# Optimization experiments

Hardware: AMD Instinct MI355X
Metric: run time of the kernel (lower is better)

Reference implementation:

```python
import jax, jax.numpy as jnp
import numpy as np

NUM_HEADS = 4
LN_EPS = 1e-5


def setup_inputs() -> dict:
    key = jax.random.key(0)
    ks = jax.random.split(key, 5)
    C = 256
    x = jax.random.normal(ks[0], (2, C, 64, 64), dtype=jnp.float32)
    in_proj_w = jax.random.normal(ks[1], (3 * C, C), dtype=jnp.float32) * (1.0 / np.sqrt(C))
    in_proj_b = jax.random.normal(ks[2], (3 * C,), dtype=jnp.float32) * 0.02
    out_w = jax.random.normal(ks[3], (C, C), dtype=jnp.float32) * (1.0 / np.sqrt(C))
    out_b = jax.random.normal(ks[4], (C,), dtype=jnp.float32) * 0.02
    ln_g = jnp.ones((C,), dtype=jnp.float32)
    ln_b = jnp.zeros((C,), dtype=jnp.float32)
    return {"x": x, "in_proj_w": in_proj_w, "in_proj_b": in_proj_b,
            "out_w": out_w, "out_b": out_b, "ln_g": ln_g, "ln_b": ln_b}


def reference(x, in_proj_w, in_proj_b, out_w, out_b, ln_g, ln_b):
    b, c, H, W = x.shape
    S = H * W  # 4096 == max_tokens -> no pooling, no interpolation
    hd = c // NUM_HEADS
    t = x.reshape(b, c, S).transpose(0, 2, 1)  # (b, S, c)
    # fused QKV projection (in_proj_weight is [3c, c], rows = q,k,v blocks)
    qkv = t @ in_proj_w.T + in_proj_b  # (b, S, 3c)
    q, k, v = jnp.split(qkv, 3, axis=-1)
    def to_heads(a):
        return a.reshape(b, S, NUM_HEADS, hd).transpose(0, 2, 1, 3)  # (b, h, S, d)
    q = to_heads(q) * (1.0 / np.sqrt(hd))
    k = to_heads(k)
    v = to_heads(v)
    scores = jnp.einsum('bhqd,bhkd->bhqk', q, k)      # (b, h, S, S)
    probs = jax.nn.softmax(scores, axis=-1)
    attn = jnp.einsum('bhqk,bhkd->bhqd', probs, v)    # (b, h, S, d)
    attn = attn.transpose(0, 2, 1, 3).reshape(b, S, c)
    out = attn @ out_w.T + out_b                      # output projection
    # LayerNorm over channel dim
    mu = jnp.mean(out, axis=-1, keepdims=True)
    var = jnp.mean(jnp.square(out - mu), axis=-1, keepdims=True)
    out = (out - mu) * jax.lax.rsqrt(var + LN_EPS) * ln_g + ln_b
    return out.transpose(0, 2, 1).reshape(b, c, H, W)
```

## Files before the change

kernel.cpp:

```cpp
#include <hip/hip_runtime.h>
#include <cstddef>

#define S_TOK 4096
#define CDIM 256
#define NHEADS 4
#define HDIM 64
#define LSK 72
#define LDA 36
#define LDY 264
#define LOG2E 1.44269504f

typedef __attribute__((ext_vector_type(8))) short short8;
typedef __attribute__((ext_vector_type(4))) float floatx4;

__device__ inline unsigned short f2bf(float f) {
  union { float f; unsigned u; } v;
  v.f = f;
  unsigned r = v.u + 0x7fff + ((v.u >> 16) & 1);
  return (unsigned short)(r >> 16);
}
__device__ inline float bf2f(unsigned short u) {
  union { unsigned u; float f; } v;
  v.u = ((unsigned)u) << 16;
  return v.f;
}
__device__ inline unsigned pack_bf16(float a, float b) {
#if __has_builtin(__builtin_amdgcn_cvt_pk_bf16_f32)
  typedef __bf16 bf16x2 __attribute__((ext_vector_type(2)));
  union { bf16x2 v; unsigned u; } r;
  r.v = __builtin_amdgcn_cvt_pk_bf16_f32(a, b);
  return r.u;
#else
  return ((unsigned)f2bf(b) << 16) | f2bf(a);
#endif
}

__global__ __launch_bounds__(256) void qkv_gemm_kernel(
    const float* __restrict__ x, const float* __restrict__ ipw,
    const float* __restrict__ ipb, unsigned short* __restrict__ q16,
    unsigned short* __restrict__ k16, unsigned short* __restrict__ vt16) {
  __shared__ __align__(16) unsigned short As[64 * LDA];
  __shared__ __align__(16) unsigned short Bs[3][64 * LDA];
  const int tid = threadIdx.x;
  const int wave = tid >> 6, lane = tid & 63;
  const int quad = lane >> 4, l16 = lane & 15;
  const int n0 = blockIdx.x * 64;
  const int tok0 = blockIdx.y * 64;
  const int b = blockIdx.z;

  const int c_l = tid >> 3, t8 = tid & 7;
  const float* gx = x + (((size_t)(b * CDIM + c_l)) << 12) + tok0 + t8 * 8;
  unsigned short* wa = &As[(t8 * 8) * LDA + c_l];

  const int rr = tid >> 2, c4 = tid & 3;
  const float* gw0 = ipw + ((size_t)(n0 + rr)) * CDIM + c4 * 8;
  unsigned short* wb0 = &Bs[0][rr * LDA + c4 * 8];

  floatx4 acc[3][4];
#pragma unroll
  for (int s = 0; s < 3; ++s)
#pragma unroll
    for (int nt = 0; nt < 4; ++nt) acc[s][nt] = (floatx4){0.f, 0.f, 0.f, 0.f};

  float4 a0 = *(const float4*)(gx);
  float4 a1 = *(const float4*)(gx + 4);
  float4 bp[3][2];
#pragma unroll
  for (int s = 0; s < 3; ++s) {
    bp[s][0] = *(const float4*)(gw0 + (size_t)s * 256 * CDIM);
    bp[s][1] = *(const float4*)(gw0 + (size_t)s * 256 * CDIM + 4);
  }

  for (int ks = 0; ks < 8; ++ks) {
    __syncthreads();
    {
      unsigned p;
      p = pack_bf16(a0.x, a0.y);
      wa[0 * LDA] = (unsigned short)p; wa[1 * LDA] = (unsigned short)(p >> 16);
      p = pack_bf16(a0.z, a0.w);
      wa[2 * LDA] = (unsigned short)p; wa[3 * LDA] = (unsigned short)(p >> 16);
      p = pack_bf16(a1.x, a1.y);
      wa[4 * LDA] = (unsigned short)p; wa[5 * LDA] = (unsigned short)(p >> 16);
      p = pack_bf16(a1.z, a1.w);
      wa[6 * LDA] = (unsigned short)p; wa[7 * LDA] = (unsigned short)(p >> 16);
    }
#pragma unroll
    for (int s = 0; s < 3; ++s) {
      uint2 u0, u1;
      u0.x = pack_bf16(bp[s][0].x, bp[s][0].y);
      u0.y = pack_bf16(bp[s][0].z, bp[s][0].w);
      u1.x = pack_bf16(bp[s][1].x, bp[s][1].y);
      u1.y = pack_bf16(bp[s][1].z, bp[s][1].w);
      unsigned short* w = wb0 + s * 64 * LDA;
      *(uint2*)w = u0;
      *(uint2*)(w + 4) = u1;
    }
    __syncthreads();
    if (ks < 7) {
      const float* gxn = gx + ((size_t)((ks + 1) * 32) << 12);
      a0 = *(const float4*)(gxn);
      a1 = *(const float4*)(gxn + 4);
#pragma unroll
      for (int s = 0; s < 3; ++s) {
        const float* g = gw0 + (size_t)s * 256 * CDIM + (ks + 1) * 32;
        bp[s][0] = *(const float4*)(g);
        bp[s][1] = *(const float4*)(g + 4);
      }
    }
    short8 af = *(const short8*)&As[(wave * 16 + l16) * LDA + quad * 8];
#pragma unroll
    for (int s = 0; s < 3; ++s)
#pragma unroll
      for (int nt = 0; nt < 4; ++nt) {
        short8 bf = *(const short8*)&Bs[s][(nt * 16 + l16) * LDA + quad * 8];
        acc[s][nt] = __builtin_amdgcn_mfma_f32_16x16x32_bf16(af, bf, acc[s][nt], 0, 0, 0);
      }
  }

  const float qsc = 0.125f * LOG2E;
#pragma unroll
  for (int nt = 0; nt < 4; ++nt) {
    int cb = n0 + nt * 16 + l16;
    int h = cb >> 6, dh = cb & 63;
    float bq = ipb[cb], bk = ipb[256 + cb], bv = ipb[512 + cb];
    size_t base = ((size_t)(b * NHEADS + h)) * S_TOK;
#pragma unroll
    for (int r = 0; r < 4; ++r) {
      int tok = tok0 + wave * 16 + quad * 4 + r;
      q16[(base + tok) * HDIM + dh] = f2bf((acc[0][nt][r] + bq) * qsc);
      k16[(base + tok) * HDIM + dh] = f2bf(acc[1][nt][r] + bk);
    }
    int tokv = tok0 + wave * 16 + quad * 4;
    uint2 u;
    u.x = pack_bf16(acc[2][nt][0] + bv, acc[2][nt][1] + bv);
    u.y = pack_bf16(acc[2][nt][2] + bv, acc[2][nt][3] + bv);
    *(uint2*)&vt16[(base * 0 + ((size_t)(b * NHEADS + h) * HDIM + dh)) * S_TOK + tokv] = u;
  }
}

__global__ __launch_bounds__(256) void attn_kernel(
    const unsigned short* __restrict__ q16,
    const unsigned short* __restrict__ k16,
    const unsigned short* __restrict__ vt16,
    unsigned short* __restrict__ op, float* __restrict__ lp) {
  __shared__ __align__(16) unsigned short Ks[64 * LSK];
  __shared__ __align__(16) unsigned short Vt[64 * LSK];
  __shared__ __align__(16) unsigned short Ps[4 * 64 * LSK];

  const int tid = threadIdx.x;
  const int wave = tid >> 6;
  const int lane = tid & 63;
  const int quad = lane >> 4;
  const int l16 = lane & 15;
  const int bh = blockIdx.y;
  const int q0 = blockIdx.x * 256;
  const int split = blockIdx.z;
  const int kt0 = split * 16;

  short8 qf[4][2];
#pragma unroll
  for (int mt = 0; mt < 4; ++mt) {
    const unsigned short* qg =
        q16 + ((size_t)bh * S_TOK + q0 + wave * 64 + mt * 16 + l16) * HDIM + quad * 8;
    qf[mt][0] = *(const short8*)(qg);
    qf[mt][1] = *(const short8*)(qg + 32);
  }

  const int sr = tid >> 3, scc = tid & 7;
  const unsigned short* kg = k16 + ((size_t)bh * S_TOK + sr) * HDIM + scc * 8;
  const unsigned short* vg = vt16 + ((size_t)bh * HDIM + sr) * S_TOK + scc * 8;
  unsigned short* ksw = &Ks[sr * LSK + scc * 8];
  unsigned short* vtw = &Vt[sr * LSK + scc * 8];

  floatx4 O[4][4];
  float lsum[4] = {0.f, 0.f, 0.f, 0.f};
#pragma unroll
  for (int mt = 0; mt < 4; ++mt)
#pragma unroll
    for (int nt = 0; nt < 4; ++nt) O[mt][nt] = (floatx4){0.f, 0.f, 0.f, 0.f};

  uint4 k0r = *(const uint4*)(kg + (size_t)kt0 * 64 * HDIM);
  uint4 k1r = *(const uint4*)(kg + (size_t)kt0 * 64 * HDIM + 32 * HDIM);
  uint4 v0r = *(const uint4*)(vg + kt0 * 64);
  uint4 v1r = *(const uint4*)(vg + kt0 * 64 + (size_t)32 * S_TOK);

  unsigned short* pw = &Ps[(wave * 64) * LSK];

  for (int t = 0; t < 16; ++t) {
    __syncthreads();
    *(uint4*)ksw = k0r;
    *(uint4*)(ksw + 32 * LSK) = k1r;
    *(uint4*)vtw = v0r;
    *(uint4*)(vtw + 32 * LSK) = v1r;
    __syncthreads();
    if (t < 15) {
      const unsigned short* kgn = kg + (size_t)(kt0 + t + 1) * 64 * HDIM;
      const unsigned short* vgn = vg + (kt0 + t + 1) * 64;
      k0r = *(const uint4*)(kgn);
      k1r = *(const uint4*)(kgn + 32 * HDIM);
      v0r = *(const uint4*)(vgn);
      v1r = *(const uint4*)(vgn + (size_t)32 * S_TOK);
    }

#pragma unroll
    for (int kt = 0; kt < 4; ++kt) {
      short8 kf0 = *(const short8*)(&Ks[(kt * 16 + l16) * LSK + quad * 8]);
      short8 kf1 = *(const short8*)(&Ks[(kt * 16 + l16) * LSK + 32 + quad * 8]);
#pragma unroll
      for (int mt = 0; mt < 4; ++mt) {
        floatx4 c = (floatx4){0.f, 0.f, 0.f, 0.f};
        c = __builtin_amdgcn_mfma_f32_16x16x32_bf16(kf0, qf[mt][0], c, 0, 0, 0);
        c = __builtin_amdgcn_mfma_f32_16x16x32_bf16(kf1, qf[mt][1], c, 0, 0, 0);
        float p0 = __builtin_amdgcn_exp2f(c[0]);
        float p1 = __builtin_amdgcn_exp2f(c[1]);
        float p2 = __builtin_amdgcn_exp2f(c[2]);
        float p3 = __builtin_amdgcn_exp2f(c[3]);
        lsum[mt] += (p0 + p1) + (p2 + p3);
        uint2 pk;
        pk.x = pack_bf16(p0, p1);
        pk.y = pack_bf16(p2, p3);
        *(uint2*)&pw[(mt * 16 + l16) * LSK + kt * 16 + quad * 4] = pk;
      }
    }

    short8 pf[4][2];
#pragma unroll
    for (int mt = 0; mt < 4; ++mt) {
      pf[mt][0] = *(const short8*)(&pw[(mt * 16 + l16) * LSK + quad * 8]);
      pf[mt][1] = *(const short8*)(&pw[(mt * 16 + l16) * LSK + 32 + quad * 8]);
    }
#pragma unroll
    for (int nt = 0; nt < 4; ++nt) {
      short8 vf0 = *(const short8*)(&Vt[(nt * 16 + l16) * LSK + quad * 8]);
      short8 vf1 = *(const short8*)(&Vt[(nt * 16 + l16) * LSK + 32 + quad * 8]);
#pragma unroll
      for (int mt = 0; mt < 4; ++mt) {
        O[mt][nt] = __builtin_amdgcn_mfma_f32_16x16x32_bf16(pf[mt][0], vf0, O[mt][nt], 0, 0, 0);
        O[mt][nt] = __builtin_amdgcn_mfma_f32_16x16x32_bf16(pf[mt][1], vf1, O[mt][nt], 0, 0, 0);
      }
    }
  }

  const int b = bh >> 2, h = bh & 3;
  unsigned short* op_s = op + (size_t)split * 2097152;
  float* lp_s = lp + (size_t)split * 32768;
#pragma unroll
  for (int mt = 0; mt < 4; ++mt) {
    float ls = lsum[mt];
    ls += __shfl_xor(ls, 16);
    ls += __shfl_xor(ls, 32);
    if (quad == 0)
      lp_s[bh * S_TOK + q0 + wave * 64 + mt * 16 + l16] = ls;
#pragma unroll
    for (int r = 0; r < 4; ++r) {
      int row = q0 + wave * 64 + mt * 16 + quad * 4 + r;
#pragma unroll
      for (int nt = 0; nt < 4; ++nt)
        op_s[((size_t)(b * S_TOK + row)) * CDIM + h * HDIM + nt * 16 + l16] =
            f2bf(O[mt][nt][r]);
    }
  }
}

__device__ inline uint2 merge4(const unsigned short* op, size_t off, float rinv) {
  float s0 = 0.f, s1 = 0.f, s2 = 0.f, s3 = 0.f;
#pragma unroll
  for (int sp = 0; sp < 4; ++sp) {
    uint2 u = *(const uint2*)(op + (size_t)sp * 2097152 + off);
    s0 += bf2f((unsigned short)(u.x & 0xffff));
    s1 += bf2f((unsigned short)(u.x >> 16));
    s2 += bf2f((unsigned short)(u.y & 0xffff));
    s3 += bf2f((unsigned short)(u.y >> 16));
  }
  uint2 r;
  r.x = pack_bf16(s0 * rinv, s1 * rinv);
  r.y = pack_bf16(s2 * rinv, s3 * rinv);
  return r;
}

__global__ __launch_bounds__(256) void out_ln_gemm_kernel(
    const unsigned short* __restrict__ op, const float* __restrict__ lp,
    const float* __restrict__ ow, const float* __restrict__ obias,
    const float* __restrict__ lng, const float* __restrict__ lnb,
    float* __restrict__ out) {
  __shared__ __align__(16) unsigned short As[32 * LDA];
  __shared__ __align__(16) unsigned short Bs[256 * LDA];
  __shared__ __align__(16) float ys[32 * LDY];
  __shared__ float rsum[128];
  const int tid = threadIdx.x;
  const int wave = tid >> 6, lane = tid & 63;
  const int quad = lane >> 4, l16 = lane & 15;
  const int tok0 = blockIdx.x * 32;

  if (tid < 128) {
    int t = tid >> 2, h = tid & 3;
    int bb = tok0 >> 12;
    int idx = (bb * 4 + h) * 4096 + (tok0 & 4095) + t;
    rsum[tid] =
        1.0f / (lp[idx] + lp[32768 + idx] + lp[65536 + idx] + lp[98304 + idx]);
  }
  __syncthreads();

  const int ar = tid >> 3, ac = tid & 7;
  const size_t abase = (size_t)(tok0 + ar) * CDIM + ac * 4;
  unsigned short* wAp = &As[ar * LDA + ac * 4];
  const int rr = tid >> 2, c4 = tid & 3;
  const float* gB = ow + (size_t)rr * CDIM + c4 * 8;
  unsigned short* wBp = &Bs[rr * LDA + c4 * 8];

  floatx4 acc[2][4];
#pragma unroll
  for (int mt = 0; mt < 2; ++mt)
#pragma unroll
    for (int nt = 0; nt < 4; ++nt) acc[mt][nt] = (floatx4){0.f, 0.f, 0.f, 0.f};

  uint2 ap = merge4(op, abase, rsum[(ar << 2) + (ac >> 4)]);
  float4 bpf[4][2];
#pragma unroll
  for (int i = 0; i < 4; ++i) {
    bpf[i][0] = *(const float4*)(gB + (size_t)i * 64 * CDIM);
    bpf[i][1] = *(const float4*)(gB + (size_t)i * 64 * CDIM + 4);
  }

  for (int ks = 0; ks < 8; ++ks) {
    __syncthreads();
    *(uint2*)wAp = ap;
#pragma unroll
    for (int i = 0; i < 4; ++i) {
      uint2 u0, u1;
      u0.x = pack_bf16(bpf[i][0].x, bpf[i][0].y);
      u0.y = pack_bf16(bpf[i][0].z, bpf[i][0].w);
      u1.x = pack_bf16(bpf[i][1].x, bpf[i][1].y);
      u1.y = pack_bf16(bpf[i][1].z, bpf[i][1].w);
      unsigned short* w = wBp + i * 64 * LDA;
      *(uint2*)w = u0;
      *(uint2*)(w + 4) = u1;
    }
    __syncthreads();
    if (ks < 7) {
      int off = (ks + 1) * 32;
      int ch = off + ac * 4;
      ap = merge4(op, abase + off, rsum[(ar << 2) + (ch >> 6)]);
#pragma unroll
      for (int i = 0; i < 4; ++i) {
        bpf[i][0] = *(const float4*)(gB + (size_t)i * 64 * CDIM + off);
        bpf[i][1] = *(const float4*)(gB + (size_t)i * 64 * CDIM + off + 4);
      }
    }
    short8 af[2], bf[4];
#pragma unroll
    for (int mt = 0; mt < 2; ++mt)
      af[mt] = *(const short8*)&As[(mt * 16 + l16) * LDA + quad * 8];
#pragma unroll
    for (int nt = 0; nt < 4; ++nt)
      bf[nt] = *(const short8*)&Bs[(wave * 64 + nt * 16 + l16) * LDA + quad * 8];
#pragma unroll
    for (int mt = 0; mt < 2; ++mt)
#pragma unroll
      for (int nt = 0; nt < 4; ++nt)
        acc[mt][nt] = __builtin_amdgcn_mfma_f32_16x16x32_bf16(af[mt], bf[nt], acc[mt][nt], 0, 0, 0);
  }

#pragma unroll
  for (int mt = 0; mt < 2; ++mt)
#pragma unroll
    for (int nt = 0; nt < 4; ++nt) {
      int c = wave * 64 + nt * 16 + l16;
      float bo = obias[c];
#pragma unroll
      for (int r = 0; r < 4; ++r)
        ys[(mt * 16 + quad * 4 + r) * LDY + c] = acc[mt][nt][r] + bo;
    }
  __syncthreads();

  const int gtok = tid >> 3, l8 = tid & 7;
  float sum = 0.f, ssq = 0.f;
#pragma unroll
  for (int i = 0; i < 32; ++i) {
    float v = ys[gtok * LDY + i * 8 + l8];
    sum += v;
    ssq += v * v;
  }
  sum += __shfl_xor(sum, 1); ssq += __shfl_xor(ssq, 1);
  sum += __shfl_xor(sum, 2); ssq += __shfl_xor(ssq, 2);
  sum += __shfl_xor(sum, 4); ssq += __shfl_xor(ssq, 4);
  float mu = sum * (1.f / 256.f);
  float var = ssq * (1.f / 256.f) - mu * mu;
  float rstd = rsqrtf(var + 1e-5f);
  const int b2 = tok0 >> 12;
  const int sl = (tok0 & 4095) + gtok;
#pragma unroll
  for (int i = 0; i < 32; ++i) {
    int c = i * 8 + l8;
    float v = ys[gtok * LDY + c];
    out[(((size_t)(b2 * CDIM + c)) << 12) + sl] = (v - mu) * rstd * lng[c] + lnb[c];
  }
}

extern "C" void kernel_launch(void* const* d_in, const int* in_sizes, int n_in,
                              void* d_out, int out_size, void* d_ws, size_t ws_size,
                              hipStream_t stream) {
  const float* x = (const float*)d_in[0];
  const float* ipw = (const float*)d_in[1];
  const float* ipb = (const float*)d_in[2];
  const float* ow = (const float*)d_in[3];
  const float* ob = (const float*)d_in[4];
  const float* lng = (const float*)d_in[5];
  const float* lnb = (const float*)d_in[6];
  float* out = (float*)d_out;
  unsigned short* q16 = (unsigned short*)d_ws;
  unsigned short* k16 = q16 + 2097152;
  unsigned short* vt16 = k16 + 2097152;
  unsigned short* op = vt16 + 2097152;
  float* lp = (float*)(op + 8388608);

  qkv_gemm_kernel<<<dim3(4, 64, 2), 256, 0, stream>>>(x, ipw, ipb, q16, k16, vt16);
  attn_kernel<<<dim3(16, 8, 4), 256, 0, stream>>>(q16, k16, vt16, op, lp);
  out_ln_gemm_kernel<<<256, 256, 0, stream>>>(op, lp, ow, ob, lng, lnb, out);
}
```

Baseline: 150.9 us.

## Keep attention probabilities in registers via permlane swaps and double-buffer K/V

The attention kernel no longer writes the exponentiated scores to a per-wave LDS buffer and reads them back as MFMA operands. It computes two 16-key score tiles, packs them to bf16 and uses v_permlane32/16_swap to rearrange them directly into the A-operand layout for the PV MFMA. K and V tiles are now double-buffered in LDS, with one barrier per iteration instead of two. The fallback pack path also switches to an inline v_cvt_pk_bf16_f32. This removes LDS traffic and a synchronisation point, but relies on gfx950-specific permlane instructions and the correctness of the lane mapping.

Measured after the change: 145.4 us. 3.7% less time.

```diff
diff --git a/kernel.cpp b/kernel.cpp
--- a/kernel.cpp
+++ b/kernel.cpp
@@ -31,8 +31,17 @@
   r.v = __builtin_amdgcn_cvt_pk_bf16_f32(a, b);
   return r.u;
 #else
-  return ((unsigned)f2bf(b) << 16) | f2bf(a);
+  unsigned r;
+  asm("v_cvt_pk_bf16_f32 %0, %1, %2" : "=v"(r) : "v"(a), "v"(b));
+  return r;
 #endif
+}
+
+__device__ inline void pl32swap(unsigned& a, unsigned& b) {
+  asm("v_permlane32_swap_b32 %0, %1" : "+v"(a), "+v"(b));
+}
+__device__ inline void pl16swap(unsigned& a, unsigned& b) {
+  asm("v_permlane16_swap_b32 %0, %1" : "+v"(a), "+v"(b));
 }
 
 __global__ __launch_bounds__(256) void qkv_gemm_kernel(
@@ -143,9 +152,8 @@
     const unsigned short* __restrict__ k16,
     const unsigned short* __restrict__ vt16,
     unsigned short* __restrict__ op, float* __restrict__ lp) {
-  __shared__ __align__(16) unsigned short Ks[64 * LSK];
-  __shared__ __align__(16) unsigned short Vt[64 * LSK];
-  __shared__ __align__(16) unsigned short Ps[4 * 64 * LSK];
+  __shared__ __align__(16) unsigned short Ks[2][64 * LSK];
+  __shared__ __align__(16) unsigned short Vt[2][64 * LSK];
 
   const int tid = threadIdx.x;
   const int wave = tid >> 6;
@@ -169,8 +177,6 @@
   const int sr = tid >> 3, scc = tid & 7;
   const unsigned short* kg = k16 + ((size_t)bh * S_TOK + sr) * HDIM + scc * 8;
   const unsigned short* vg = vt16 + ((size_t)bh * HDIM + sr) * S_TOK + scc * 8;
-  unsigned short* ksw = &Ks[sr * LSK + scc * 8];
-  unsigned short* vtw = &Vt[sr * LSK + scc * 8];
 
   floatx4 O[4][4];
   float lsum[4] = {0.f, 0.f, 0.f, 0.f};
@@ -183,16 +189,18 @@
   uint4 k1r = *(const uint4*)(kg + (size_t)kt0 * 64 * HDIM + 32 * HDIM);
   uint4 v0r = *(const uint4*)(vg + kt0 * 64);
   uint4 v1r = *(const uint4*)(vg + kt0 * 64 + (size_t)32 * S_TOK);
-
-  unsigned short* pw = &Ps[(wave * 64) * LSK];
+  {
+    unsigned short* kw = &Ks[0][sr * LSK + scc * 8];
+    unsigned short* vw = &Vt[0][sr * LSK + scc * 8];
+    *(uint4*)kw = k0r;
+    *(uint4*)(kw + 32 * LSK) = k1r;
+    *(uint4*)vw = v0r;
+    *(uint4*)(vw + 32 * LSK) = v1r;
+  }
+  __syncthreads();
 
   for (int t = 0; t < 16; ++t) {
-    __syncthreads();
-    *(uint4*)ksw = k0r;
-    *(uint4*)(ksw + 32 * LSK) = k1r;
-    *(uint4*)vtw = v0r;
-    *(uint4*)(vtw + 32 * LSK) = v1r;
-    __syncthreads();
+    const int cur = t & 1;
     if (t < 15) {
       const unsigned short* kgn = kg + (size_t)(kt0 + t + 1) * 64 * HDIM;
       const unsigned short* vgn = vg + (kt0 + t + 1) * 64;
@@ -201,43 +209,56 @@
       v0r = *(const uint4*)(vgn);
       v1r = *(const uint4*)(vgn + (size_t)32 * S_TOK);
     }
-
-#pragma unroll
-    for (int kt = 0; kt < 4; ++kt) {
-      short8 kf0 = *(const short8*)(&Ks[(kt * 16 + l16) * LSK + quad * 8]);
-      short8 kf1 = *(const short8*)(&Ks[(kt * 16 + l16) * LSK + 32 + quad * 8]);
+    const unsigned short* Kb = Ks[cur];
+    const unsigned short* Vb = Vt[cur];
+
+#pragma unroll
+    for (int c = 0; c < 2; ++c) {
+      short8 kfA0 = *(const short8*)(&Kb[((c * 2) * 16 + l16) * LSK + quad * 8]);
+      short8 kfA1 = *(const short8*)(&Kb[((c * 2) * 16 + l16) * LSK + 32 + quad * 8]);
+      short8 kfB0 = *(const short8*)(&Kb[((c * 2 + 1) * 16 + l16) * LSK + quad * 8]);
+      short8 kfB1 = *(const short8*)(&Kb[((c * 2 + 1) * 16 + l16) * LSK + 32 + quad * 8]);
+      short8 vf[4];
+#pragma unroll
+      for (int nt = 0; nt < 4; ++nt)
+        vf[nt] = *(const short8*)(&Vb[(nt * 16 + l16) * LSK + c * 32 + quad * 8]);
 #pragma unroll
       for (int mt = 0; mt < 4; ++mt) {
-        floatx4 c = (floatx4){0.f, 0.f, 0.f, 0.f};
-        c = __builtin_amdgcn_mfma_f32_16x16x32_bf16(kf0, qf[mt][0], c, 0, 0, 0);
-        c = __builtin_amdgcn_mfma_f32_16x16x32_bf16(kf1, qf[mt][1], c, 0, 0, 0);
-        float p0 = __builtin_amdgcn_exp2f(c[0]);
-        float p1 = __builtin_amdgcn_exp2f(c[1]);
-        float p2 = __builtin_amdgcn_exp2f(c[2]);
-        float p3 = __builtin_amdgcn_exp2f(c[3]);
-        lsum[mt] += (p0 + p1) + (p2 + p3);
-        uint2 pk;
-        pk.x = pack_bf16(p0, p1);
-        pk.y = pack_bf16(p2, p3);
-        *(uint2*)&pw[(mt * 16 + l16) * LSK + kt * 16 + quad * 4] = pk;
+        floatx4 cA = (floatx4){0.f, 0.f, 0.f, 0.f};
+        cA = __builtin_amdgcn_mfma_f32_16x16x32_bf16(kfA0, qf[mt][0], cA, 0, 0, 0);
+        cA = __builtin_amdgcn_mfma_f32_16x16x32_bf16(kfA1, qf[mt][1], cA, 0, 0, 0);
+        floatx4 cB = (floatx4){0.f, 0.f, 0.f, 0.f};
+        cB = __builtin_amdgcn_mfma_f32_16x16x32_bf16(kfB0, qf[mt][0], cB, 0, 0, 0);
+        cB = __builtin_amdgcn_mfma_f32_16x16x32_bf16(kfB1, qf[mt][1], cB, 0, 0, 0);
+        float a0 = __builtin_amdgcn_exp2f(cA[0]);
+        float a1 = __builtin_amdgcn_exp2f(cA[1]);
+        float a2 = __builtin_amdgcn_exp2f(cA[2]);
+        float a3 = __builtin_amdgcn_exp2f(cA[3]);
+        float b0 = __builtin_amdgcn_exp2f(cB[0]);
+        float b1 = __builtin_amdgcn_exp2f(cB[1]);
+        float b2 = __builtin_amdgcn_exp2f(cB[2]);
+        float b3 = __builtin_amdgcn_exp2f(cB[3]);
+        lsum[mt] += ((a0 + a1) + (a2 + a3)) + ((b0 + b1) + (b2 + b3));
+        unsigned A0 = pack_bf16(a0, a1), B0 = pack_bf16(a2, a3);
+        unsigned A1 = pack_bf16(b0, b1), B1 = pack_bf16(b2, b3);
+        pl32swap(A0, A1); pl16swap(A0, A1);
+        pl32swap(B0, B1); pl16swap(B0, B1);
+        union { uint4 u; short8 s; } pf;
+        pf.u.x = A0; pf.u.y = B0; pf.u.z = A1; pf.u.w = B1;
+#pragma unroll
+        for (int nt = 0; nt < 4; ++nt)
+          O[mt][nt] = __builtin_amdgcn_mfma_f32_16x16x32_bf16(pf.s, vf[nt], O[mt][nt], 0, 0, 0);
       }
     }
 
-    short8 pf[4][2];
-#pragma unroll
-    for (int mt = 0; mt < 4; ++mt) {
-      pf[mt][0] = *(const short8*)(&pw[(mt * 16 + l16) * LSK + quad * 8]);
-      pf[mt][1] = *(const short8*)(&pw[(mt * 16 + l16) * LSK + 32 + quad * 8]);
-    }
-#pragma unroll
-    for (int nt = 0; nt < 4; ++nt) {
-      short8 vf0 = *(const short8*)(&Vt[(nt * 16 + l16) * LSK + quad * 8]);
-      short8 vf1 = *(const short8*)(&Vt[(nt * 16 + l16) * LSK + 32 + quad * 8]);
-#pragma unroll
-      for (int mt = 0; mt < 4; ++mt) {
-        O[mt][nt] = __builtin_amdgcn_mfma_f32_16x16x32_bf16(pf[mt][0], vf0, O[mt][nt], 0, 0, 0);
-        O[mt][nt] = __builtin_amdgcn_mfma_f32_16x16x32_bf16(pf[mt][1], vf1, O[mt][nt], 0, 0, 0);
-      }
+    if (t < 15) {
+      unsigned short* kw = &Ks[cur ^ 1][sr * LSK + scc * 8];
+      unsigned short* vw = &Vt[cur ^ 1][sr * LSK + scc * 8];
+      *(uint4*)kw = k0r;
+      *(uint4*)(kw + 32 * LSK) = k1r;
+      *(uint4*)vw = v0r;
+      *(uint4*)(vw + 32 * LSK) = v1r;
+      __syncthreads();
     }
   }
 
```
